# Optimization experiments

Measured on AMD Instinct MI355X. Metric: run time of the kernel, lower is better.

## Reference

```python
import jax, jax.numpy as jnp
import numpy as np

H = 128   # hidden_dim (d_model)
N = 64    # SSM state size (S4D default)
OUT = 1   # output_dim


def setup_inputs() -> dict:
    key = jax.random.key(0)
    ks = jax.random.split(key, 8)
    B, L = 32, 4096
    data = jax.random.normal(ks[0], (B, L, 1), dtype=jnp.float32)
    # input projector Linear(1, H)
    W_in = jax.random.normal(ks[1], (1, H), dtype=jnp.float32) * 0.5
    b_in = jnp.zeros((H,), dtype=jnp.float32)
    # S4D SSM parameters (per-channel diagonal state space)
    rng = np.random.default_rng(0)
    log_dt = jnp.asarray(np.log(0.001) + rng.random(H) * (np.log(0.1) - np.log(0.001)), dtype=jnp.float32)
    log_A_real = jnp.full((H, N), np.log(0.5), dtype=jnp.float32)
    A_imag = jnp.asarray(np.pi * np.broadcast_to(np.arange(N), (H, N)), dtype=jnp.float32)
    C_re = jax.random.normal(ks[2], (H, N), dtype=jnp.float32) * (0.5 ** 0.5)
    C_im = jax.random.normal(ks[3], (H, N), dtype=jnp.float32) * (0.5 ** 0.5)
    D = jax.random.normal(ks[4], (H,), dtype=jnp.float32)
    # S4Block position-wise output linear with GLU: Linear(H, 2H) -> glu -> H
    W_glu = jax.random.normal(ks[5], (H, 2 * H), dtype=jnp.float32) * (1.0 / H ** 0.5)
    b_glu = jnp.zeros((2 * H,), dtype=jnp.float32)
    # output projector Linear(H, OUT)
    W_out = jax.random.normal(ks[6], (H, OUT), dtype=jnp.float32) * (1.0 / H ** 0.5)
    b_out = jnp.zeros((OUT,), dtype=jnp.float32)
    return dict(data=data, W_in=W_in, b_in=b_in, log_dt=log_dt,
                log_A_real=log_A_real, A_imag=A_imag, C_re=C_re, C_im=C_im, D=D,
                W_glu=W_glu, b_glu=b_glu, W_out=W_out, b_out=b_out)


def reference(data, W_in, b_in, log_dt, log_A_real, A_imag, C_re, C_im, D,
              W_glu, b_glu, W_out, b_out):
    # input projection: [B, L, 1] -> [B, L, H]
    u = data @ W_in + b_in
    B, L, Hh = u.shape
    # --- S4D kernel (ZOH discretization) ---
    dt = jnp.exp(log_dt)                             # (H,)
    A = -jnp.exp(log_A_real) + 1j * A_imag           # (H, N) complex64
    dtA = dt[:, None] * A                            # (H, N)
    C = C_re + 1j * C_im                             # (H, N)
    Bt = C * (jnp.exp(dtA) - 1.0) / A                # (H, N)
    l = jnp.arange(L, dtype=jnp.float32)
    vand = jnp.exp(dtA[:, :, None] * l)              # (H, N, L) Vandermonde
    K = 2.0 * jnp.einsum('hn,hnl->hl', Bt, vand).real  # (H, L) conv kernel
    # --- causal convolution via FFT ---
    n = 2 * L
    Kf = jnp.fft.rfft(K, n=n, axis=-1)               # (H, n//2+1)
    Uf = jnp.fft.rfft(u, n=n, axis=1)                # (B, n//2+1, H)
    y = jnp.fft.irfft(Uf * Kf.T[None], n=n, axis=1)[:, :L, :]
    y = y + u * D                                    # skip connection D*u
    # --- S4Block post: activation + GLU output linear (dropout off / eval) ---
    y = jax.nn.gelu(y)
    z = y @ W_glu + b_glu                            # (B, L, 2H)
    y = z[..., :Hh] * jax.nn.sigmoid(z[..., Hh:])    # GLU -> (B, L, H)
    # hidden = last-step representation, reshaped to (B, H)
    hidden = y[:, -1, :]
    out = hidden @ W_out + b_out                     # (B, OUT)
    return out  # final_activ is identity (activ_type=None)
```

## Files before the change

### kernel.cpp

```cpp
#include <hip/hip_runtime.h>
#include <math.h>

constexpr int Hd = 128;
constexpr int Nd = 64;
constexpr int Ld = 4096;
constexpr int Bd = 32;
constexpr int PARTS = 8;
constexpr int WIN   = Ld / PARTS;
constexpr int NL    = WIN / 64;

__device__ __forceinline__ float fracf(float x) { return x - floorf(x); }

__global__ __launch_bounds__(512, 8) void k_fused(
    const float* __restrict__ log_dt,
    const float* __restrict__ log_A_real,
    const float* __restrict__ A_imag,
    const float* __restrict__ C_re,
    const float* __restrict__ C_im,
    const float* __restrict__ data,
    float* __restrict__ partS,
    float* __restrict__ partK)
{
    const int bid  = blockIdx.x;
    const int h    = bid >> 3;
    const int part = bid & 7;
    const int t    = threadIdx.x;
    const int base = part * WIN;

    __shared__ float sC[Nd][8];
    __shared__ float sKp[8][WIN];
    __shared__ float sK[WIN];
    __shared__ float sKs[8];

    if (t < Nd) {
        const int n = t;
        float dt   = expf(log_dt[h]);
        float a_re = -expf(log_A_real[h*Nd + n]);
        float a_im = A_imag[h*Nd + n];
        float dre  = dt * a_re, dim = dt * a_im;
        float er1 = expf(dre);
        float s1, c1; sincosf(dim, &s1, &c1);
        float em1_re = er1*c1 - 1.0f;
        float em1_im = er1*s1;
        float inv  = 1.0f / (a_re*a_re + a_im*a_im);
        float q_re = (em1_re*a_re + em1_im*a_im) * inv;
        float q_im = (em1_im*a_re - em1_re*a_im) * inv;
        float cre = C_re[h*Nd + n], cim = C_im[h*Nd + n];
        float btr = cre*q_re - cim*q_im;
        float bti = cre*q_im + cim*q_re;

        float  dreL2 = dre * 1.4426950408889634f;
        double rev   = (double)dt * (double)a_im * 0.15915494309189535;
        double fb_d  = rev * (double)base;  fb_d -= floor(fb_d);
        double f1_d  = rev - floor(rev);
        float  er64 = exp2f(dreL2 * 64.0f);
        double p64  = rev * 64.0;  p64 -= floor(p64);
        float  fp   = (float)p64;
        float  Sr = er64 * __builtin_amdgcn_cosf(fp);
        float  Si = er64 * __builtin_amdgcn_sinf(fp);

        sC[n][0] = btr;   sC[n][1] = bti;         sC[n][2] = Sr;          sC[n][3] = Si;
        sC[n][4] = dreL2; sC[n][5] = (float)fb_d; sC[n][6] = (float)f1_d; sC[n][7] = 0.f;
    }
    __syncthreads();

    const int wv   = t >> 6;
    const int lane = t & 63;
    const int n0   = wv * 8;
    const float lbf = (float)lane;
    const float l0f = (float)(base + lane);

    float acc[NL];
    #pragma unroll
    for (int j = 0; j < NL; ++j) acc[j] = 0.f;

    #pragma unroll
    for (int n = n0; n < n0 + 8; ++n) {
        float4 cA = *(const float4*)&sC[n][0];
        float4 cB = *(const float4*)&sC[n][4];
        float er = exp2f(cB.x * l0f);
        float ph = fracf(fmaf(cB.z, lbf, cB.y));
        float sn = __builtin_amdgcn_sinf(ph);
        float cs = __builtin_amdgcn_cosf(ph);
        float pr = er*cs, pi = er*sn;
        float u  = cA.x*pr - cA.y*pi;
        float v  = cA.x*pi + cA.y*pr;
        float c1 = cA.z + cA.z;
        float c2 = -fmaf(cA.z, cA.z, cA.w*cA.w);
        float x0 = u;
        float x1 = fmaf(u, cA.z, -(v*cA.w));
        acc[0] += x0;  acc[1] += x1;
        #pragma unroll
        for (int j = 2; j < NL; ++j) {
            float x2 = fmaf(c1, x1, c2*x0);
            acc[j] += x2;
            x0 = x1;  x1 = x2;
        }
    }

    #pragma unroll
    for (int j = 0; j < NL; ++j) sKp[wv][lane + 64*j] = acc[j];

    float ksl = 0.f;
    #pragma unroll
    for (int j = 0; j < NL; ++j) ksl += acc[j];
    ksl *= 2.0f;
    #pragma unroll
    for (int off = 32; off >= 1; off >>= 1) ksl += __shfl_xor(ksl, off);
    if (lane == 0) sKs[wv] = ksl;
    __syncthreads();
    if (t == 0) {
        float pk = 0.f;
        #pragma unroll
        for (int g = 0; g < 8; ++g) pk += sKs[g];
        partK[bid] = pk;
    }

    if (t < WIN/4) {
        float4 r = make_float4(0.f, 0.f, 0.f, 0.f);
        #pragma unroll
        for (int g = 0; g < 8; ++g) {
            float4 a = ((const float4*)sKp[g])[t];
            r.x += a.x; r.y += a.y; r.z += a.z; r.w += a.w;
        }
        r.x *= 2.0f; r.y *= 2.0f; r.z *= 2.0f; r.w *= 2.0f;
        ((float4*)sK)[t] = r;
    }
    __syncthreads();

    float4 xva[4], xvb[4];
    #pragma unroll
    for (int bi = 0; bi < 4; ++bi) {
        const float* xb = data + (size_t)(wv*4 + bi)*Ld + (Ld - 4 - base);
        xva[bi] = *(const float4*)(xb - 4*lane);
        xvb[bi] = *(const float4*)(xb - 4*(lane + 64));
    }
    const float4* sK4 = (const float4*)sK;
    float4 k0 = sK4[lane], k1 = sK4[lane + 64];
    #pragma unroll
    for (int bi = 0; bi < 4; ++bi) {
        float s = k0.x*xva[bi].w + k0.y*xva[bi].z + k0.z*xva[bi].y + k0.w*xva[bi].x
                + k1.x*xvb[bi].w + k1.y*xvb[bi].z + k1.z*xvb[bi].y + k1.w*xvb[bi].x;
        #pragma unroll
        for (int off = 32; off >= 1; off >>= 1) s += __shfl_xor(s, off);
        if (lane == 0) partS[(size_t)(wv*4 + bi)*(Hd*PARTS) + bid] = s;
    }
}

__global__ __launch_bounds__(512) void k_tail(
    const float* __restrict__ data,
    const float* __restrict__ partS,
    const float* __restrict__ partK,
    const float* __restrict__ W_in,
    const float* __restrict__ b_in,
    const float* __restrict__ Dvec,
    const float* __restrict__ W_glu,
    const float* __restrict__ b_glu,
    const float* __restrict__ W_out,
    const float* __restrict__ b_out,
    float* __restrict__ out)
{
    const int b    = blockIdx.x;
    const int t    = threadIdx.x;
    const int j    = t & 255;
    const int half = t >> 8;
    __shared__ float sy[Hd];
    __shared__ float szp[2][2*Hd];
    __shared__ float sred[2];

    if (t < Hd) {
        const int hh = t;
        const float4* ps4 = (const float4*)(partS + (size_t)b*(Hd*PARTS) + hh*PARTS);
        const float4* pk4 = (const float4*)(partK + hh*PARTS);
        float4 s0 = ps4[0], s1 = ps4[1], k0 = pk4[0], k1 = pk4[1];
        float s  = s0.x+s0.y+s0.z+s0.w + s1.x+s1.y+s1.z+s1.w;
        float ks = k0.x+k0.y+k0.z+k0.w + k1.x+k1.y+k1.z+k1.w;
        float w  = W_in[hh], bi2 = b_in[hh];
        float ulast = data[(size_t)b*Ld + (Ld - 1)] * w + bi2;
        float y  = w*s + bi2*ks + ulast*Dvec[hh];
        float arg = 0.7978845608028654f*(y + 0.044715f*y*y*y);
        float e2  = __expf(2.0f*arg);
        float th  = 1.0f - 2.0f/(e2 + 1.0f);
        sy[hh] = 0.5f*y*(1.0f + th);
    }
    __syncthreads();

    float zz = half ? 0.0f : b_glu[j];
    const int h0 = half * 64;
    #pragma unroll 16
    for (int hh = h0; hh < h0 + 64; ++hh)
        zz += sy[hh] * W_glu[hh*(2*Hd) + j];
    szp[half][j] = zz;
    __syncthreads();

    float g = 0.0f;
    if (t < Hd) {
        float zl = szp[0][t]      + szp[1][t];
        float zh = szp[0][t + Hd] + szp[1][t + Hd];
        float sig = 1.0f / (1.0f + __expf(-zh));
        g = zl * sig * W_out[t];
    }
    if (t < 2*Hd) {
        #pragma unroll
        for (int off = 32; off >= 1; off >>= 1) g += __shfl_xor(g, off);
        if ((t & 63) == 0) sred[t >> 6] = g;
    }
    __syncthreads();
    if (t == 0) out[b] = sred[0] + sred[1] + b_out[0];
}

extern "C" void kernel_launch(void* const* d_in, const int* in_sizes, int n_in,
                              void* d_out, int out_size, void* d_ws, size_t ws_size,
                              hipStream_t stream) {
    const float* data   = (const float*)d_in[0];
    const float* W_in   = (const float*)d_in[1];
    const float* b_in   = (const float*)d_in[2];
    const float* log_dt = (const float*)d_in[3];
    const float* log_A  = (const float*)d_in[4];
    const float* A_im   = (const float*)d_in[5];
    const float* C_re   = (const float*)d_in[6];
    const float* C_im   = (const float*)d_in[7];
    const float* Dvec   = (const float*)d_in[8];
    const float* W_glu  = (const float*)d_in[9];
    const float* b_glu  = (const float*)d_in[10];
    const float* W_out  = (const float*)d_in[11];
    const float* b_out  = (const float*)d_in[12];
    float* out = (float*)d_out;

    float* partS = (float*)d_ws;
    float* partK = partS + (size_t)Bd*Hd*PARTS;

    k_fused<<<dim3(Hd*PARTS), 512, 0, stream>>>(log_dt, log_A, A_im, C_re, C_im,
                                                data, partS, partK);
    k_tail <<<Bd, 512, 0, stream>>>(data, partS, partK, W_in, b_in, Dvec,
                                    W_glu, b_glu, W_out, b_out, out);
}
```

Baseline: 17.50 us.

## Fuse tail into main kernel using global atomic counter completion barrier

Merges the two kernels into one: every block increments a global counter after writing its partial sums, and the first Bd blocks spin until all blocks have finished, then run the GELU/GLU/output tail. This removes the second kernel launch and its inter-kernel gap, but adds a memset of the counter, a spin-wait that depends on all blocks being co-resident, and relies on relaxed atomics for cross-block visibility.

```diff
diff --git a/kernel.cpp b/kernel.cpp
--- a/kernel.cpp
+++ b/kernel.cpp
@@ -8,18 +8,28 @@
 constexpr int PARTS = 8;
 constexpr int WIN   = Ld / PARTS;
 constexpr int NL    = WIN / 64;
+constexpr int NBLK  = Hd * PARTS;
 
 __device__ __forceinline__ float fracf(float x) { return x - floorf(x); }
 
-__global__ __launch_bounds__(512, 8) void k_fused(
+__global__ __launch_bounds__(512, 8) void k_all(
+    const float* __restrict__ data,
+    const float* __restrict__ W_in,
+    const float* __restrict__ b_in,
     const float* __restrict__ log_dt,
     const float* __restrict__ log_A_real,
     const float* __restrict__ A_imag,
     const float* __restrict__ C_re,
     const float* __restrict__ C_im,
-    const float* __restrict__ data,
+    const float* __restrict__ Dvec,
+    const float* __restrict__ W_glu,
+    const float* __restrict__ b_glu,
+    const float* __restrict__ W_out,
+    const float* __restrict__ b_out,
     float* __restrict__ partS,
-    float* __restrict__ partK)
+    float* __restrict__ partK,
+    unsigned* __restrict__ counter,
+    float* __restrict__ out)
 {
     const int bid  = blockIdx.x;
     const int h    = bid >> 3;
@@ -31,6 +41,9 @@
     __shared__ float sKp[8][WIN];
     __shared__ float sK[WIN];
     __shared__ float sKs[8];
+    __shared__ float sy[Hd];
+    __shared__ float szp[2][2*Hd];
+    __shared__ float sred[2];
 
     if (t < Nd) {
         const int n = t;
@@ -113,7 +126,7 @@
         float pk = 0.f;
         #pragma unroll
         for (int g = 0; g < 8; ++g) pk += sKs[g];
-        partK[bid] = pk;
+        __hip_atomic_store(&partK[bid], pk, __ATOMIC_RELAXED, __HIP_MEMORY_SCOPE_AGENT);
     }
 
     if (t < WIN/4) {
@@ -143,38 +156,37 @@
                 + k1.x*xvb[bi].w + k1.y*xvb[bi].z + k1.z*xvb[bi].y + k1.w*xvb[bi].x;
         #pragma unroll
         for (int off = 32; off >= 1; off >>= 1) s += __shfl_xor(s, off);
-        if (lane == 0) partS[(size_t)(wv*4 + bi)*(Hd*PARTS) + bid] = s;
-    }
-}
-
-__global__ __launch_bounds__(512) void k_tail(
-    const float* __restrict__ data,
-    const float* __restrict__ partS,
-    const float* __restrict__ partK,
-    const float* __restrict__ W_in,
-    const float* __restrict__ b_in,
-    const float* __restrict__ Dvec,
-    const float* __restrict__ W_glu,
-    const float* __restrict__ b_glu,
-    const float* __restrict__ W_out,
-    const float* __restrict__ b_out,
-    float* __restrict__ out)
-{
-    const int b    = blockIdx.x;
-    const int t    = threadIdx.x;
-    const int j    = t & 255;
+        if (lane == 0)
+            __hip_atomic_store(&partS[(size_t)(wv*4 + bi)*NBLK + bid], s,
+                               __ATOMIC_RELAXED, __HIP_MEMORY_SCOPE_AGENT);
+    }
+
+    __syncthreads();
+    if (t == 0)
+        __hip_atomic_fetch_add(counter, 1u, __ATOMIC_RELAXED, __HIP_MEMORY_SCOPE_AGENT);
+    if (bid >= Bd) return;
+
+    if (t == 0) {
+        while (__hip_atomic_load(counter, __ATOMIC_RELAXED, __HIP_MEMORY_SCOPE_AGENT)
+               < (unsigned)NBLK)
+            __builtin_amdgcn_s_sleep(1);
+    }
+    __syncthreads();
+
+    const int b = bid;
+    const int j = t & 255;
     const int half = t >> 8;
-    __shared__ float sy[Hd];
-    __shared__ float szp[2][2*Hd];
-    __shared__ float sred[2];
 
     if (t < Hd) {
         const int hh = t;
-        const float4* ps4 = (const float4*)(partS + (size_t)b*(Hd*PARTS) + hh*PARTS);
-        const float4* pk4 = (const float4*)(partK + hh*PARTS);
-        float4 s0 = ps4[0], s1 = ps4[1], k0 = pk4[0], k1 = pk4[1];
-        float s  = s0.x+s0.y+s0.z+s0.w + s1.x+s1.y+s1.z+s1.w;
-        float ks = k0.x+k0.y+k0.z+k0.w + k1.x+k1.y+k1.z+k1.w;
+        float s = 0.f, ks = 0.f;
+        #pragma unroll
+        for (int p = 0; p < PARTS; ++p) {
+            s  += __hip_atomic_load(&partS[(size_t)b*NBLK + hh*PARTS + p],
+                                    __ATOMIC_RELAXED, __HIP_MEMORY_SCOPE_AGENT);
+            ks += __hip_atomic_load(&partK[hh*PARTS + p],
+                                    __ATOMIC_RELAXED, __HIP_MEMORY_SCOPE_AGENT);
+        }
         float w  = W_in[hh], bi2 = b_in[hh];
         float ulast = data[(size_t)b*Ld + (Ld - 1)] * w + bi2;
         float y  = w*s + bi2*ks + ulast*Dvec[hh];
@@ -227,11 +239,12 @@
     const float* b_out  = (const float*)d_in[12];
     float* out = (float*)d_out;
 
-    float* partS = (float*)d_ws;
-    float* partK = partS + (size_t)Bd*Hd*PARTS;
-
-    k_fused<<<dim3(Hd*PARTS), 512, 0, stream>>>(log_dt, log_A, A_im, C_re, C_im,
-                                                data, partS, partK);
-    k_tail <<<Bd, 512, 0, stream>>>(data, partS, partK, W_in, b_in, Dvec,
-                                    W_glu, b_glu, W_out, b_out, out);
+    float*    partS   = (float*)d_ws;
+    float*    partK   = partS + (size_t)Bd*NBLK;
+    unsigned* counter = (unsigned*)(partK + NBLK);
+
+    hipMemsetAsync(counter, 0, sizeof(unsigned), stream);
+    k_all<<<NBLK, 512, 0, stream>>>(data, W_in, b_in, log_dt, log_A, A_im,
+                                    C_re, C_im, Dvec, W_glu, b_glu, W_out, b_out,
+                                    partS, partK, counter, out);
 }
```

Result: slower. 47.91 us (+173.7%).
